# Kernel tuning notes

Hardware: AMD Instinct MI355X
Metric: run time of the kernel (lower is better)

Reference implementation:

```python
import jax, jax.numpy as jnp
import numpy as np

B, S, NX, NH = 2, 2048, 1024, 16
HD = NX // NH  # head dim = 64

def setup_inputs() -> dict:
    key = jax.random.key(0)
    k1, k2, k3 = jax.random.split(key, 3)
    return {
        "x": jax.random.normal(k1, (B, S, NX), dtype=jnp.float32),
        "c_attn_w": jax.random.normal(k2, (NX, 3 * NX), dtype=jnp.float32) * 0.02,
        "c_attn_b": jnp.zeros((3 * NX,), dtype=jnp.float32),
        "c_proj_w": jax.random.normal(k3, (NX, NX), dtype=jnp.float32) * 0.02,
        "c_proj_b": jnp.zeros((NX,), dtype=jnp.float32),
    }

def reference(x, c_attn_w, c_attn_b, c_proj_w, c_proj_b):
    b, s, nx = x.shape
    # fused QKV projection (Conv1D == affine on last dim)
    qkv = x @ c_attn_w + c_attn_b                      # [b, s, 3*nx]
    q, k, v = jnp.split(qkv, 3, axis=-1)
    # split heads -> [b, h, s, d]
    q = q.reshape(b, s, NH, HD).transpose(0, 2, 1, 3)
    k = k.reshape(b, s, NH, HD).transpose(0, 2, 1, 3)
    v = v.reshape(b, s, NH, HD).transpose(0, 2, 1, 3)
    # scaled scores with causal mask (masked_fill -1e10, matching original)
    w = jnp.einsum("bhqd,bhkd->bhqk", q, k) / jnp.sqrt(jnp.float32(HD))
    causal = jnp.tril(jnp.ones((s, s), dtype=bool))    # [s, s]
    w = jnp.where(causal[None, None, :, :], w, jnp.float32(-1e10))
    w = jax.nn.softmax(w, axis=-1)
    a = jnp.einsum("bhqk,bhkd->bhqd", w, v)            # [b, h, s, d]
    # merge heads
    a = a.transpose(0, 2, 1, 3).reshape(b, s, nx)
    # output projection (dropout is identity in eval)
    return a @ c_proj_w + c_proj_b
```

## Files before the change

kernel.cpp:

```cpp
#include <hip/hip_runtime.h>
#include <cstdint>

typedef unsigned short u16;
typedef unsigned int u32;
typedef float f32x4 __attribute__((ext_vector_type(4)));
typedef __bf16 bf16x8 __attribute__((ext_vector_type(8)));
typedef __bf16 bf16x4 __attribute__((ext_vector_type(4)));
typedef u16 u16x8 __attribute__((ext_vector_type(8)));

#define B_ 2
#define S_ 2048
#define NX_ 1024
#define NH_ 16
#define HD_ 64
#define T3_ 3072
#define M_ 4096
#define SCL 0.18033688011112042f

__device__ __forceinline__ u16 bfbits(float f) {
    __bf16 h = (__bf16)f;
    return __builtin_bit_cast(u16, h);
}

__device__ __forceinline__ void gload_lds16(const void* g, void* l) {
    auto gp = reinterpret_cast<const __attribute__((address_space(1))) u32*>(
        reinterpret_cast<uintptr_t>(g));
    auto lp = reinterpret_cast<__attribute__((address_space(3))) u32*>(
        reinterpret_cast<uintptr_t>(l));
    __builtin_amdgcn_global_load_lds(gp, lp, 16, 0, 0);
}

__global__ __launch_bounds__(256) void cvt_bf16_kernel(const float* __restrict__ X,
                                                       u16* __restrict__ Y) {
    int i = (blockIdx.x * 256 + threadIdx.x) * 4;
    float4 v = *reinterpret_cast<const float4*>(X + i);
    bf16x4 o;
    o[0] = (__bf16)v.x; o[1] = (__bf16)v.y; o[2] = (__bf16)v.z; o[3] = (__bf16)v.w;
    *reinterpret_cast<bf16x4*>(Y + i) = o;
}

__global__ __launch_bounds__(256) void transpose_cvt_kernel(const float* __restrict__ W,
                                                            u16* __restrict__ WT,
                                                            int K, int N) {
    __shared__ float tile[32][33];
    int nbx = N >> 5;
    int nb = (blockIdx.x % nbx) << 5;
    int kb = (blockIdx.x / nbx) << 5;
    int tx = threadIdx.x & 31, ty = threadIdx.x >> 5;
#pragma unroll
    for (int i = 0; i < 32; i += 8)
        tile[ty + i][tx] = W[(size_t)(kb + ty + i) * N + nb + tx];
    __syncthreads();
#pragma unroll
    for (int i = 0; i < 32; i += 8)
        WT[(size_t)(nb + ty + i) * K + kb + tx] = bfbits(tile[tx][ty + i]);
}

#define BM 128
#define BN 128
#define BK 64
__global__ __launch_bounds__(256) void gemm_bt_kernel(const u16* __restrict__ A,
                                                      const u16* __restrict__ Bt,
                                                      const float* __restrict__ bias,
                                                      u16* __restrict__ Cb,
                                                      float* __restrict__ Cf,
                                                      u16* __restrict__ Vt,
                                                      int vcol0,
                                                      int M, int N, int K) {
    __shared__ u16 a_lds[BM * BK];
    __shared__ u16 b_lds[BN * BK];
    int nbn = N / BN;
    int nwg = gridDim.x;
    int orig = blockIdx.x;
    int wg = (orig & 7) * (nwg >> 3) + (orig >> 3);
    int bm = wg / nbn, bn = wg % nbn;
    int t = threadIdx.x;
    int w = t >> 6, l = t & 63, lg = l >> 4, lr = l & 15;
    int wr = w >> 1, wc = w & 1;
    const u16* Abase = A + (size_t)bm * BM * K;
    const u16* Bbase = Bt + (size_t)bn * BN * K;

    f32x4 zero4 = {0.f, 0.f, 0.f, 0.f};
    f32x4 acc[4][4];
#pragma unroll
    for (int m = 0; m < 4; ++m)
#pragma unroll
        for (int n = 0; n < 4; ++n) acc[m][n] = zero4;

    int nkt = K / BK;
    for (int kt = 0; kt < nkt; ++kt) {
#pragma unroll
        for (int it = 0; it < 4; ++it) {
            int idx = it * 256 + t;
            int row = idx >> 3, ck = idx & 7;
            int ldsoff = (it * 256 + w * 64) * 8;
            gload_lds16(Abase + (size_t)row * K + kt * BK + ck * 8, a_lds + ldsoff);
            gload_lds16(Bbase + (size_t)row * K + kt * BK + ck * 8, b_lds + ldsoff);
        }
        __syncthreads();
#pragma unroll
        for (int ks = 0; ks < 2; ++ks) {
            bf16x8 af[4], bf[4];
#pragma unroll
            for (int m = 0; m < 4; ++m)
                af[m] = *reinterpret_cast<const bf16x8*>(
                    a_lds + (wr * 64 + m * 16 + lr) * BK + ks * 32 + lg * 8);
#pragma unroll
            for (int n = 0; n < 4; ++n)
                bf[n] = *reinterpret_cast<const bf16x8*>(
                    b_lds + (wc * 64 + n * 16 + lr) * BK + ks * 32 + lg * 8);
#pragma unroll
            for (int m = 0; m < 4; ++m)
#pragma unroll
                for (int n = 0; n < 4; ++n)
                    acc[m][n] = __builtin_amdgcn_mfma_f32_16x16x32_bf16(
                        af[m], bf[n], acc[m][n], 0, 0, 0);
        }
        __syncthreads();
    }
#pragma unroll
    for (int n = 0; n < 4; ++n) {
        int col0 = bn * BN + wc * 64 + n * 16;
        int col = col0 + lr;
        float bv = bias[col];
        bool isv = (Vt != nullptr) && (col0 >= vcol0);
#pragma unroll
        for (int m = 0; m < 4; ++m) {
            int row0 = bm * BM + wr * 64 + m * 16 + lg * 4;
            if (isv) {
                int nv = col - vcol0, hh = nv >> 6, dd = nv & 63;
                int bb = row0 >> 11, ss = row0 & 2047;
                bf16x4 pk;
#pragma unroll
                for (int r = 0; r < 4; ++r) pk[r] = (__bf16)(acc[m][n][r] + bv);
                *reinterpret_cast<bf16x4*>(
                    Vt + (((size_t)(bb * 16 + hh) * 64 + dd) << 11) + ss) = pk;
            } else {
#pragma unroll
                for (int r = 0; r < 4; ++r) {
                    float v = acc[m][n][r] + bv;
                    if (Cf) Cf[(size_t)(row0 + r) * N + col] = v;
                    else    Cb[(size_t)(row0 + r) * N + col] = bfbits(v);
                }
            }
        }
    }
}

__global__ __launch_bounds__(256) void attn_kernel(const u16* __restrict__ qkv,
                                                   const u16* __restrict__ Vt,
                                                   u16* __restrict__ outa) {
    __shared__ u16 k_lds[2][4096];
    __shared__ u16 v_lds[2][4096];
    __shared__ u16 p_lds[4096];

    int bid = blockIdx.x;
    int g = bid & 31;
    int j = bid >> 5;
    int j0 = j & 7, kk = j >> 3;
    int qt = (kk == 0) ? j0 : (kk == 1) ? (31 - j0) : (kk == 2) ? (8 + j0) : (23 - j0);
    int b = g >> 4, h = g & 15;
    int t = threadIdx.x, w = t >> 6, l = t & 63, lg = l >> 4, lr = l & 15;
    const u16* base = qkv + (size_t)b * S_ * T3_;
    const u16* vbase = Vt + (size_t)g * 64 * S_;
    int prow = w * 16 + lr;
    int srow = w * 8 + (l >> 3);
    int qb = qt * 64;
    int qrow = qb + w * 16 + lr;

    auto stage = [&](int kt2, int bs) {
        int kb2 = kt2 * 64;
#pragma unroll
        for (int it = 0; it < 2; ++it) {
            int row = it * 32 + srow;
            int ckg = (l & 7) ^ (row & 7);
            gload_lds16(base + (size_t)(kb2 + row) * T3_ + NX_ + h * 64 + ckg * 8,
                        &k_lds[bs][(it * 32 + w * 8) * 64]);
            gload_lds16(vbase + (size_t)row * S_ + kb2 + ckg * 8,
                        &v_lds[bs][(it * 32 + w * 8) * 64]);
        }
    };

    f32x4 zero4 = {0.f, 0.f, 0.f, 0.f};

    bf16x8 qf[2];
#pragma unroll
    for (int ks = 0; ks < 2; ++ks)
        qf[ks] = *reinterpret_cast<const bf16x8*>(
            base + (size_t)qrow * T3_ + h * 64 + ks * 32 + lg * 8);

    f32x4 oacc[4];
#pragma unroll
    for (int dc = 0; dc < 4; ++dc) oacc[dc] = zero4;
    float mrun = -1e30f, lrun = 0.f;
    int nkt = qt + 1;

    stage(0, 0);
    __syncthreads();

    for (int kt = 0; kt < nkt; ++kt) {
        int cur = kt & 1;
        if (kt + 1 < nkt) stage(kt + 1, cur ^ 1);

        f32x4 sacc[4];
#pragma unroll
        for (int kn = 0; kn < 4; ++kn) sacc[kn] = zero4;
        __builtin_amdgcn_s_setprio(1);
#pragma unroll
        for (int ks = 0; ks < 2; ++ks) {
#pragma unroll
            for (int kn = 0; kn < 4; ++kn) {
                bf16x8 kf = *reinterpret_cast<const bf16x8*>(
                    &k_lds[cur][(kn * 16 + lr) * 64 + (((ks * 4 + lg) ^ (lr & 7)) * 8)]);
                sacc[kn] = __builtin_amdgcn_mfma_f32_16x16x32_bf16(
                    kf, qf[ks], sacc[kn], 0, 0, 0);
            }
        }
        __builtin_amdgcn_s_setprio(0);

        if (kt == qt) {
            int qloc = w * 16 + lr;
#pragma unroll
            for (int kn = 0; kn < 4; ++kn)
#pragma unroll
                for (int r = 0; r < 4; ++r)
                    if (kn * 16 + lg * 4 + r > qloc) sacc[kn][r] = -1e30f;
        }

        float mx = -1e30f;
#pragma unroll
        for (int kn = 0; kn < 4; ++kn) {
            float a0 = fmaxf(sacc[kn][0], sacc[kn][1]);
            float a1 = fmaxf(sacc[kn][2], sacc[kn][3]);
            mx = fmaxf(mx, fmaxf(a0, a1));
        }
        mx = fmaxf(mx, __shfl_xor(mx, 16));
        mx = fmaxf(mx, __shfl_xor(mx, 32));

        bool noresc = __all(mx <= mrun + 8.0f);
        float mnew = noresc ? mrun : fmaxf(mrun, mx);

        float rs = 0.f;
#pragma unroll
        for (int kn = 0; kn < 4; ++kn)
#pragma unroll
            for (int r = 0; r < 4; ++r) {
                float pv = exp2f((sacc[kn][r] - mnew) * SCL);
                sacc[kn][r] = pv;
                rs += pv;
            }
        rs += __shfl_xor(rs, 16);
        rs += __shfl_xor(rs, 32);

        if (noresc) {
            lrun += rs;
        } else {
            float fsc = exp2f((mrun - mnew) * SCL);
            mrun = mnew;
            lrun = lrun * fsc + rs;
            float f0 = __shfl(fsc, lg * 4 + 0);
            float f1 = __shfl(fsc, lg * 4 + 1);
            float f2 = __shfl(fsc, lg * 4 + 2);
            float f3 = __shfl(fsc, lg * 4 + 3);
#pragma unroll
            for (int dc = 0; dc < 4; ++dc) {
                oacc[dc][0] *= f0; oacc[dc][1] *= f1;
                oacc[dc][2] *= f2; oacc[dc][3] *= f3;
            }
        }

#pragma unroll
        for (int kn = 0; kn < 4; ++kn) {
            bf16x4 pb;
            pb[0] = (__bf16)sacc[kn][0]; pb[1] = (__bf16)sacc[kn][1];
            pb[2] = (__bf16)sacc[kn][2]; pb[3] = (__bf16)sacc[kn][3];
            int byteoff = prow * 128 + (((2 * kn + (lg >> 1)) ^ (prow & 7)) * 16) + (lg & 1) * 8;
            *reinterpret_cast<bf16x4*>(reinterpret_cast<char*>(p_lds) + byteoff) = pb;
        }

        __builtin_amdgcn_s_setprio(1);
#pragma unroll
        for (int ks = 0; ks < 2; ++ks) {
            bf16x8 pf = *reinterpret_cast<const bf16x8*>(
                reinterpret_cast<char*>(p_lds) + prow * 128 + (((ks * 4 + lg) ^ (prow & 7)) * 16));
#pragma unroll
            for (int dc = 0; dc < 4; ++dc) {
                bf16x8 vf = *reinterpret_cast<const bf16x8*>(
                    &v_lds[cur][(dc * 16 + lr) * 64 + (((ks * 4 + lg) ^ (lr & 7)) * 8)]);
                oacc[dc] = __builtin_amdgcn_mfma_f32_16x16x32_bf16(
                    pf, vf, oacc[dc], 0, 0, 0);
            }
        }
        __builtin_amdgcn_s_setprio(0);
        __syncthreads();
    }

    float inv = 1.f / lrun;
    float i0 = __shfl(inv, lg * 4 + 0);
    float i1 = __shfl(inv, lg * 4 + 1);
    float i2 = __shfl(inv, lg * 4 + 2);
    float i3 = __shfl(inv, lg * 4 + 3);
    u16* ob = outa + (size_t)b * S_ * NX_;
#pragma unroll
    for (int r = 0; r < 4; ++r) {
        float ir = (r == 0) ? i0 : (r == 1) ? i1 : (r == 2) ? i2 : i3;
        int row = qb + w * 16 + lg * 4 + r;
#pragma unroll
        for (int dc = 0; dc < 4; ++dc)
            ob[(size_t)row * NX_ + h * 64 + dc * 16 + lr] = bfbits(oacc[dc][r] * ir);
    }
}

extern "C" void kernel_launch(void* const* d_in, const int* in_sizes, int n_in,
                              void* d_out, int out_size, void* d_ws, size_t ws_size,
                              hipStream_t stream) {
    const float* x        = (const float*)d_in[0];
    const float* c_attn_w = (const float*)d_in[1];
    const float* c_attn_b = (const float*)d_in[2];
    const float* c_proj_w = (const float*)d_in[3];
    const float* c_proj_b = (const float*)d_in[4];
    float* out = (float*)d_out;

    u16* xb     = (u16*)d_ws;
    u16* wqkvT  = xb + (size_t)M_ * NX_;
    u16* wprojT = wqkvT + (size_t)T3_ * NX_;
    u16* qkv    = wprojT + (size_t)NX_ * NX_;
    u16* attno  = xb;
    u16* Vtp    = (u16*)d_out;

    cvt_bf16_kernel<<<(M_ * NX_) / 1024, 256, 0, stream>>>(x, xb);
    transpose_cvt_kernel<<<(T3_ / 32) * (NX_ / 32), 256, 0, stream>>>(c_attn_w, wqkvT, NX_, T3_);
    transpose_cvt_kernel<<<(NX_ / 32) * (NX_ / 32), 256, 0, stream>>>(c_proj_w, wprojT, NX_, NX_);
    gemm_bt_kernel<<<(M_ / BM) * (T3_ / BN), 256, 0, stream>>>(
        xb, wqkvT, c_attn_b, qkv, nullptr, Vtp, 2 * NX_, M_, T3_, NX_);
    attn_kernel<<<1024, 256, 0, stream>>>(qkv, Vtp, attno);
    gemm_bt_kernel<<<(M_ / BM) * (NX_ / BN), 256, 0, stream>>>(
        attno, wprojT, c_proj_b, nullptr, out, nullptr, 0, M_, NX_, NX_);
}
```

Measured before the change: 127.9 us.

## Rewrite attention with 32x32x16 MFMA, 128-row query tiles, register P exchange

The attention kernel now gives each block a 128-row query tile, with each wave owning 32 rows, and uses 32x32x16 bf16 MFMA for both QK^T and PV. The P matrix is repacked in registers with lane shuffles instead of a round trip through LDS, which removes the p_lds buffer. Each K/V tile loaded into LDS is now reused by twice as many query rows, and the grid is halved with a simpler causal tile ordering. In exchange, waves with fewer causal tiles sit idle in the later iterations while still hitting the barriers, and register pressure rises with the larger accumulators.

```diff
diff --git a/kernel.cpp b/kernel.cpp
--- a/kernel.cpp
+++ b/kernel.cpp
@@ -4,9 +4,12 @@
 typedef unsigned short u16;
 typedef unsigned int u32;
 typedef float f32x4 __attribute__((ext_vector_type(4)));
+typedef float f32x16 __attribute__((ext_vector_type(16)));
 typedef __bf16 bf16x8 __attribute__((ext_vector_type(8)));
 typedef __bf16 bf16x4 __attribute__((ext_vector_type(4)));
+typedef __bf16 bf16x2 __attribute__((ext_vector_type(2)));
 typedef u16 u16x8 __attribute__((ext_vector_type(8)));
+typedef u32 u32x4 __attribute__((ext_vector_type(4)));
 
 #define B_ 2
 #define S_ 2048
@@ -20,6 +23,10 @@
 __device__ __forceinline__ u16 bfbits(float f) {
     __bf16 h = (__bf16)f;
     return __builtin_bit_cast(u16, h);
+}
+__device__ __forceinline__ u32 pk2(float a, float b) {
+    bf16x2 t; t[0] = (__bf16)a; t[1] = (__bf16)b;
+    return __builtin_bit_cast(u32, t);
 }
 
 __device__ __forceinline__ void gload_lds16(const void* g, void* l) {
@@ -152,21 +159,19 @@
                                                    u16* __restrict__ outa) {
     __shared__ u16 k_lds[2][4096];
     __shared__ u16 v_lds[2][4096];
-    __shared__ u16 p_lds[4096];
 
     int bid = blockIdx.x;
     int g = bid & 31;
     int j = bid >> 5;
-    int j0 = j & 7, kk = j >> 3;
-    int qt = (kk == 0) ? j0 : (kk == 1) ? (31 - j0) : (kk == 2) ? (8 + j0) : (23 - j0);
+    int qt = (j < 8) ? (15 - j) : (j - 8);
     int b = g >> 4, h = g & 15;
-    int t = threadIdx.x, w = t >> 6, l = t & 63, lg = l >> 4, lr = l & 15;
+    int t = threadIdx.x, w = t >> 6, l = t & 63;
+    int c31 = l & 31, hi = l >> 5;
     const u16* base = qkv + (size_t)b * S_ * T3_;
     const u16* vbase = Vt + (size_t)g * 64 * S_;
-    int prow = w * 16 + lr;
     int srow = w * 8 + (l >> 3);
-    int qb = qt * 64;
-    int qrow = qb + w * 16 + lr;
+    int qb = qt * 128 + w * 32;
+    int q = qb + c31;
 
     auto stage = [&](int kt2, int bs) {
         int kb2 = kt2 * 64;
@@ -181,19 +186,21 @@
         }
     };
 
-    f32x4 zero4 = {0.f, 0.f, 0.f, 0.f};
-
-    bf16x8 qf[2];
-#pragma unroll
-    for (int ks = 0; ks < 2; ++ks)
+    bf16x8 qf[4];
+#pragma unroll
+    for (int ks = 0; ks < 4; ++ks)
         qf[ks] = *reinterpret_cast<const bf16x8*>(
-            base + (size_t)qrow * T3_ + h * 64 + ks * 32 + lg * 8);
-
-    f32x4 oacc[4];
-#pragma unroll
-    for (int dc = 0; dc < 4; ++dc) oacc[dc] = zero4;
+            base + (size_t)q * T3_ + h * 64 + ks * 16 + hi * 8);
+
+    f32x16 oacc[2];
+#pragma unroll
+    for (int dc = 0; dc < 2; ++dc)
+#pragma unroll
+        for (int r = 0; r < 16; ++r) oacc[dc][r] = 0.f;
     float mrun = -1e30f, lrun = 0.f;
-    int nkt = qt + 1;
+
+    int nkt = 2 * qt + 2;
+    int tw = 2 * qt + (w >> 1);
 
     stage(0, 0);
     __syncthreads();
@@ -202,112 +209,121 @@
         int cur = kt & 1;
         if (kt + 1 < nkt) stage(kt + 1, cur ^ 1);
 
-        f32x4 sacc[4];
-#pragma unroll
-        for (int kn = 0; kn < 4; ++kn) sacc[kn] = zero4;
-        __builtin_amdgcn_s_setprio(1);
-#pragma unroll
-        for (int ks = 0; ks < 2; ++ks) {
-#pragma unroll
-            for (int kn = 0; kn < 4; ++kn) {
-                bf16x8 kf = *reinterpret_cast<const bf16x8*>(
-                    &k_lds[cur][(kn * 16 + lr) * 64 + (((ks * 4 + lg) ^ (lr & 7)) * 8)]);
-                sacc[kn] = __builtin_amdgcn_mfma_f32_16x16x32_bf16(
-                    kf, qf[ks], sacc[kn], 0, 0, 0);
-            }
-        }
-        __builtin_amdgcn_s_setprio(0);
-
-        if (kt == qt) {
-            int qloc = w * 16 + lr;
-#pragma unroll
-            for (int kn = 0; kn < 4; ++kn)
-#pragma unroll
-                for (int r = 0; r < 4; ++r)
-                    if (kn * 16 + lg * 4 + r > qloc) sacc[kn][r] = -1e30f;
-        }
-
-        float mx = -1e30f;
-#pragma unroll
-        for (int kn = 0; kn < 4; ++kn) {
-            float a0 = fmaxf(sacc[kn][0], sacc[kn][1]);
-            float a1 = fmaxf(sacc[kn][2], sacc[kn][3]);
-            mx = fmaxf(mx, fmaxf(a0, a1));
-        }
-        mx = fmaxf(mx, __shfl_xor(mx, 16));
-        mx = fmaxf(mx, __shfl_xor(mx, 32));
-
-        bool noresc = __all(mx <= mrun + 8.0f);
-        float mnew = noresc ? mrun : fmaxf(mrun, mx);
-
-        float rs = 0.f;
-#pragma unroll
-        for (int kn = 0; kn < 4; ++kn)
-#pragma unroll
-            for (int r = 0; r < 4; ++r) {
-                float pv = exp2f((sacc[kn][r] - mnew) * SCL);
-                sacc[kn][r] = pv;
-                rs += pv;
-            }
-        rs += __shfl_xor(rs, 16);
-        rs += __shfl_xor(rs, 32);
-
-        if (noresc) {
-            lrun += rs;
-        } else {
-            float fsc = exp2f((mrun - mnew) * SCL);
-            mrun = mnew;
-            lrun = lrun * fsc + rs;
-            float f0 = __shfl(fsc, lg * 4 + 0);
-            float f1 = __shfl(fsc, lg * 4 + 1);
-            float f2 = __shfl(fsc, lg * 4 + 2);
-            float f3 = __shfl(fsc, lg * 4 + 3);
-#pragma unroll
-            for (int dc = 0; dc < 4; ++dc) {
-                oacc[dc][0] *= f0; oacc[dc][1] *= f1;
-                oacc[dc][2] *= f2; oacc[dc][3] *= f3;
-            }
-        }
-
-#pragma unroll
-        for (int kn = 0; kn < 4; ++kn) {
-            bf16x4 pb;
-            pb[0] = (__bf16)sacc[kn][0]; pb[1] = (__bf16)sacc[kn][1];
-            pb[2] = (__bf16)sacc[kn][2]; pb[3] = (__bf16)sacc[kn][3];
-            int byteoff = prow * 128 + (((2 * kn + (lg >> 1)) ^ (prow & 7)) * 16) + (lg & 1) * 8;
-            *reinterpret_cast<bf16x4*>(reinterpret_cast<char*>(p_lds) + byteoff) = pb;
-        }
-
-        __builtin_amdgcn_s_setprio(1);
-#pragma unroll
-        for (int ks = 0; ks < 2; ++ks) {
-            bf16x8 pf = *reinterpret_cast<const bf16x8*>(
-                reinterpret_cast<char*>(p_lds) + prow * 128 + (((ks * 4 + lg) ^ (prow & 7)) * 16));
-#pragma unroll
-            for (int dc = 0; dc < 4; ++dc) {
-                bf16x8 vf = *reinterpret_cast<const bf16x8*>(
-                    &v_lds[cur][(dc * 16 + lr) * 64 + (((ks * 4 + lg) ^ (lr & 7)) * 8)]);
-                oacc[dc] = __builtin_amdgcn_mfma_f32_16x16x32_bf16(
-                    pf, vf, oacc[dc], 0, 0, 0);
-            }
-        }
-        __builtin_amdgcn_s_setprio(0);
+        if (kt <= tw) {
+            int kb = kt * 64;
+            f32x16 sacc[2];
+#pragma unroll
+            for (int kn = 0; kn < 2; ++kn)
+#pragma unroll
+                for (int r = 0; r < 16; ++r) sacc[kn][r] = 0.f;
+            __builtin_amdgcn_s_setprio(1);
+#pragma unroll
+            for (int ks = 0; ks < 4; ++ks) {
+#pragma unroll
+                for (int kn = 0; kn < 2; ++kn) {
+                    int row = kn * 32 + c31;
+                    int ck = (ks * 2 + hi) ^ (row & 7);
+                    bf16x8 kf = *reinterpret_cast<const bf16x8*>(
+                        &k_lds[cur][row * 64 + ck * 8]);
+                    sacc[kn] = __builtin_amdgcn_mfma_f32_32x32x16_bf16(
+                        kf, qf[ks], sacc[kn], 0, 0, 0);
+                }
+            }
+            __builtin_amdgcn_s_setprio(0);
+
+            if (kt == tw) {
+#pragma unroll
+                for (int kn = 0; kn < 2; ++kn)
+#pragma unroll
+                    for (int r = 0; r < 16; ++r) {
+                        int kv = kb + kn * 32 + (r & 3) + 8 * (r >> 2) + 4 * hi;
+                        if (kv > q) sacc[kn][r] = -1e30f;
+                    }
+            }
+
+            float mx = -1e30f;
+#pragma unroll
+            for (int kn = 0; kn < 2; ++kn)
+#pragma unroll
+                for (int r = 0; r < 16; ++r) mx = fmaxf(mx, sacc[kn][r]);
+            mx = fmaxf(mx, __shfl_xor(mx, 32));
+
+            bool noresc = __all(mx <= mrun + 8.0f);
+            float mnew = noresc ? mrun : fmaxf(mrun, mx);
+
+            float rs = 0.f;
+#pragma unroll
+            for (int kn = 0; kn < 2; ++kn)
+#pragma unroll
+                for (int r = 0; r < 16; ++r) {
+                    float pv = exp2f((sacc[kn][r] - mnew) * SCL);
+                    sacc[kn][r] = pv;
+                    rs += pv;
+                }
+            rs += __shfl_xor(rs, 32);
+
+            if (noresc) {
+                lrun += rs;
+            } else {
+                float fsc = exp2f((mrun - mnew) * SCL);
+                mrun = mnew;
+                lrun = lrun * fsc + rs;
+#pragma unroll
+                for (int r = 0; r < 16; ++r) {
+                    int cr = (r & 3) + 8 * (r >> 2) + 4 * hi;
+                    float f = __shfl(fsc, cr);
+                    oacc[0][r] *= f; oacc[1][r] *= f;
+                }
+            }
+
+            __builtin_amdgcn_s_setprio(1);
+#pragma unroll
+            for (int kn = 0; kn < 2; ++kn) {
+                u32 a0 = pk2(sacc[kn][0],  sacc[kn][1]),  a1 = pk2(sacc[kn][2],  sacc[kn][3]);
+                u32 b0 = pk2(sacc[kn][4],  sacc[kn][5]),  b1 = pk2(sacc[kn][6],  sacc[kn][7]);
+                u32 c0 = pk2(sacc[kn][8],  sacc[kn][9]),  c1 = pk2(sacc[kn][10], sacc[kn][11]);
+                u32 d0 = pk2(sacc[kn][12], sacc[kn][13]), d1 = pk2(sacc[kn][14], sacc[kn][15]);
+                u32 pa0 = __shfl_xor(a0, 32), pa1 = __shfl_xor(a1, 32);
+                u32 pb0 = __shfl_xor(b0, 32), pb1 = __shfl_xor(b1, 32);
+                u32 pc0 = __shfl_xor(c0, 32), pc1 = __shfl_xor(c1, 32);
+                u32 pd0 = __shfl_xor(d0, 32), pd1 = __shfl_xor(d1, 32);
+                u32x4 f0, f1;
+                f0[0] = hi ? pb0 : a0;  f0[1] = hi ? pb1 : a1;
+                f0[2] = hi ? b0 : pa0;  f0[3] = hi ? b1 : pa1;
+                f1[0] = hi ? pd0 : c0;  f1[1] = hi ? pd1 : c1;
+                f1[2] = hi ? d0 : pc0;  f1[3] = hi ? d1 : pc1;
+                bf16x8 pf0 = __builtin_bit_cast(bf16x8, f0);
+                bf16x8 pf1 = __builtin_bit_cast(bf16x8, f1);
+#pragma unroll
+                for (int dc = 0; dc < 2; ++dc) {
+                    int d = dc * 32 + c31;
+                    int ck0 = ((kn * 2 + 0) * 2 + hi) ^ (d & 7);
+                    int ck1 = ((kn * 2 + 1) * 2 + hi) ^ (d & 7);
+                    bf16x8 vf0 = *reinterpret_cast<const bf16x8*>(
+                        &v_lds[cur][d * 64 + ck0 * 8]);
+                    oacc[dc] = __builtin_amdgcn_mfma_f32_32x32x16_bf16(
+                        pf0, vf0, oacc[dc], 0, 0, 0);
+                    bf16x8 vf1 = *reinterpret_cast<const bf16x8*>(
+                        &v_lds[cur][d * 64 + ck1 * 8]);
+                    oacc[dc] = __builtin_amdgcn_mfma_f32_32x32x16_bf16(
+                        pf1, vf1, oacc[dc], 0, 0, 0);
+                }
+            }
+            __builtin_amdgcn_s_setprio(0);
+        }
         __syncthreads();
     }
 
     float inv = 1.f / lrun;
-    float i0 = __shfl(inv, lg * 4 + 0);
-    float i1 = __shfl(inv, lg * 4 + 1);
-    float i2 = __shfl(inv, lg * 4 + 2);
-    float i3 = __shfl(inv, lg * 4 + 3);
     u16* ob = outa + (size_t)b * S_ * NX_;
 #pragma unroll
-    for (int r = 0; r < 4; ++r) {
-        float ir = (r == 0) ? i0 : (r == 1) ? i1 : (r == 2) ? i2 : i3;
-        int row = qb + w * 16 + lg * 4 + r;
-#pragma unroll
-        for (int dc = 0; dc < 4; ++dc)
-            ob[(size_t)row * NX_ + h * 64 + dc * 16 + lr] = bfbits(oacc[dc][r] * ir);
+    for (int r = 0; r < 16; ++r) {
+        int cr = (r & 3) + 8 * (r >> 2) + 4 * hi;
+        float iv = __shfl(inv, cr);
+        int row = qb + cr;
+#pragma unroll
+        for (int dc = 0; dc < 2; ++dc)
+            ob[(size_t)row * NX_ + h * 64 + dc * 32 + c31] = bfbits(oacc[dc][r] * iv);
     }
 }
 
@@ -333,7 +349,7 @@
     transpose_cvt_kernel<<<(NX_ / 32) * (NX_ / 32), 256, 0, stream>>>(c_proj_w, wprojT, NX_, NX_);
     gemm_bt_kernel<<<(M_ / BM) * (T3_ / BN), 256, 0, stream>>>(
         xb, wqkvT, c_attn_b, qkv, nullptr, Vtp, 2 * NX_, M_, T3_, NX_);
-    attn_kernel<<<1024, 256, 0, stream>>>(qkv, Vtp, attno);
+    attn_kernel<<<512, 256, 0, stream>>>(qkv, Vtp, attno);
     gemm_bt_kernel<<<(M_ / BM) * (NX_ / BN), 256, 0, stream>>>(
         attno, wprojT, c_proj_b, nullptr, out, nullptr, 0, M_, NX_, NX_);
 }
```

Measured after the change: 138.9 us. +8.6%, slower.

## Split causal attention KV range across two blocks and merge partial results

Applied to the files above, without the earlier changes.

Each query tile's key range is now split into two halves handled by separate blocks, doubling the attention grid. Tiles are scheduled longest-first. Each block writes unnormalized partial outputs plus its running max and sum into spare workspace regions. A new merge kernel rescales and combines the two partials into the final attention output. The aim is shorter per-block critical paths and better CU balance across the causal triangle, paid for with an extra kernel launch and extra global memory traffic for the partials.

```diff
diff --git a/kernel.cpp b/kernel.cpp
--- a/kernel.cpp
+++ b/kernel.cpp
@@ -149,7 +149,9 @@
 
 __global__ __launch_bounds__(256) void attn_kernel(const u16* __restrict__ qkv,
                                                    const u16* __restrict__ Vt,
-                                                   u16* __restrict__ outa) {
+                                                   u16* __restrict__ part0,
+                                                   u16* __restrict__ part1,
+                                                   float* __restrict__ mlb) {
     __shared__ u16 k_lds[2][4096];
     __shared__ u16 v_lds[2][4096];
     __shared__ u16 p_lds[4096];
@@ -157,8 +159,8 @@
     int bid = blockIdx.x;
     int g = bid & 31;
     int j = bid >> 5;
-    int j0 = j & 7, kk = j >> 3;
-    int qt = (kk == 0) ? j0 : (kk == 1) ? (31 - j0) : (kk == 2) ? (8 + j0) : (23 - j0);
+    int qt = 31 - (j >> 1);
+    int s = j & 1;
     int b = g >> 4, h = g & 15;
     int t = threadIdx.x, w = t >> 6, l = t & 63, lg = l >> 4, lr = l & 15;
     const u16* base = qkv + (size_t)b * S_ * T3_;
@@ -168,6 +170,11 @@
     int qb = qt * 64;
     int qrow = qb + w * 16 + lr;
 
+    int nt = qt + 1;
+    int h1 = (nt + 1) >> 1;
+    int k0 = s ? h1 : 0;
+    int k1 = s ? nt : h1;
+
     auto stage = [&](int kt2, int bs) {
         int kb2 = kt2 * 64;
 #pragma unroll
@@ -193,14 +200,13 @@
 #pragma unroll
     for (int dc = 0; dc < 4; ++dc) oacc[dc] = zero4;
     float mrun = -1e30f, lrun = 0.f;
-    int nkt = qt + 1;
-
-    stage(0, 0);
+
+    if (k0 < k1) stage(k0, 0);
     __syncthreads();
 
-    for (int kt = 0; kt < nkt; ++kt) {
-        int cur = kt & 1;
-        if (kt + 1 < nkt) stage(kt + 1, cur ^ 1);
+    for (int kt = k0; kt < k1; ++kt) {
+        int cur = (kt - k0) & 1;
+        if (kt + 1 < k1) stage(kt + 1, cur ^ 1);
 
         f32x4 sacc[4];
 #pragma unroll
@@ -295,19 +301,42 @@
         __syncthreads();
     }
 
-    float inv = 1.f / lrun;
-    float i0 = __shfl(inv, lg * 4 + 0);
-    float i1 = __shfl(inv, lg * 4 + 1);
-    float i2 = __shfl(inv, lg * 4 + 2);
-    float i3 = __shfl(inv, lg * 4 + 3);
-    u16* ob = outa + (size_t)b * S_ * NX_;
+    u16* pb = (s ? part1 : part0) + (size_t)b * S_ * NX_;
 #pragma unroll
     for (int r = 0; r < 4; ++r) {
-        float ir = (r == 0) ? i0 : (r == 1) ? i1 : (r == 2) ? i2 : i3;
         int row = qb + w * 16 + lg * 4 + r;
 #pragma unroll
         for (int dc = 0; dc < 4; ++dc)
-            ob[(size_t)row * NX_ + h * 64 + dc * 16 + lr] = bfbits(oacc[dc][r] * ir);
+            pb[(size_t)row * NX_ + h * 64 + dc * 16 + lr] = bfbits(oacc[dc][r]);
+    }
+    if (lg == 0) {
+        float* f = mlb + (size_t)(b * S_ + qrow) * (T3_ / 2) + (NX_ / 2) * 2 + h * 4 + s * 2;
+        f[0] = mrun; f[1] = lrun;
+    }
+}
+
+__global__ __launch_bounds__(256) void merge_kernel(u16* __restrict__ part0,
+                                                    const u16* __restrict__ part1,
+                                                    const float* __restrict__ mlb) {
+    int idx = blockIdx.x * 256 + threadIdx.x;
+    int tok = idx >> 4, h = idx & 15;
+    const float* f = mlb + (size_t)tok * (T3_ / 2) + (NX_ / 2) * 2 + h * 4;
+    float m0 = f[0], l0 = f[1], m1 = f[2], l1 = f[3];
+    float M = fmaxf(m0, m1);
+    float e0 = exp2f((m0 - M) * SCL), e1 = exp2f((m1 - M) * SCL);
+    float inv = 1.f / (l0 * e0 + l1 * e1);
+    float a = e0 * inv, c = e1 * inv;
+    u16* p0 = part0 + (size_t)tok * NX_ + h * 64;
+    const u16* p1 = part1 + (size_t)tok * NX_ + h * 64;
+#pragma unroll
+    for (int i = 0; i < 8; ++i) {
+        bf16x8 v0 = *reinterpret_cast<const bf16x8*>(p0 + i * 8);
+        bf16x8 v1 = *reinterpret_cast<const bf16x8*>(p1 + i * 8);
+        bf16x8 o;
+#pragma unroll
+        for (int k = 0; k < 8; ++k)
+            o[k] = (__bf16)((float)v0[k] * a + (float)v1[k] * c);
+        *reinterpret_cast<bf16x8*>(p0 + i * 8) = o;
     }
 }
 
@@ -327,13 +356,16 @@
     u16* qkv    = wprojT + (size_t)NX_ * NX_;
     u16* attno  = xb;
     u16* Vtp    = (u16*)d_out;
+    u16* part1  = Vtp + (size_t)32 * 64 * S_;
+    float* mlb  = (float*)qkv;
 
     cvt_bf16_kernel<<<(M_ * NX_) / 1024, 256, 0, stream>>>(x, xb);
     transpose_cvt_kernel<<<(T3_ / 32) * (NX_ / 32), 256, 0, stream>>>(c_attn_w, wqkvT, NX_, T3_);
     transpose_cvt_kernel<<<(NX_ / 32) * (NX_ / 32), 256, 0, stream>>>(c_proj_w, wprojT, NX_, NX_);
     gemm_bt_kernel<<<(M_ / BM) * (T3_ / BN), 256, 0, stream>>>(
         xb, wqkvT, c_attn_b, qkv, nullptr, Vtp, 2 * NX_, M_, T3_, NX_);
-    attn_kernel<<<1024, 256, 0, stream>>>(qkv, Vtp, attno);
+    attn_kernel<<<2048, 256, 0, stream>>>(qkv, Vtp, attno, part1, mlb);
+    merge_kernel<<<(M_ * NH_) / 256, 256, 0, stream>>>(attno, part1, mlb);
     gemm_bt_kernel<<<(M_ / BM) * (NX_ / BN), 256, 0, stream>>>(
         attno, wprojT, c_proj_b, nullptr, out, nullptr, 0, M_, NX_, NX_);
 }
```

After: 132.7 us. +3.8%, slower.

## Load K and V fragments directly from global memory instead of staging through LDS

Applied to the files above, without the earlier changes.

The attention kernel drops its double-buffered LDS staging of K and V tiles. Each wave now reads its MFMA fragments straight from global memory (relying on L2/L1 caching) and removes the per-iteration block barrier. Launch bounds are raised to request higher occupancy. The trade is that each of the four waves redundantly fetches the same K/V tiles and there is no explicit prefetch, so global-load latency is exposed inside the loop.

```diff
diff --git a/kernel.cpp b/kernel.cpp
--- a/kernel.cpp
+++ b/kernel.cpp
@@ -147,11 +147,9 @@
     }
 }
 
-__global__ __launch_bounds__(256) void attn_kernel(const u16* __restrict__ qkv,
-                                                   const u16* __restrict__ Vt,
-                                                   u16* __restrict__ outa) {
-    __shared__ u16 k_lds[2][4096];
-    __shared__ u16 v_lds[2][4096];
+__global__ __launch_bounds__(256, 4) void attn_kernel(const u16* __restrict__ qkv,
+                                                      const u16* __restrict__ Vt,
+                                                      u16* __restrict__ outa) {
     __shared__ u16 p_lds[4096];
 
     int bid = blockIdx.x;
@@ -164,22 +162,11 @@
     const u16* base = qkv + (size_t)b * S_ * T3_;
     const u16* vbase = Vt + (size_t)g * 64 * S_;
     int prow = w * 16 + lr;
-    int srow = w * 8 + (l >> 3);
     int qb = qt * 64;
     int qrow = qb + w * 16 + lr;
 
-    auto stage = [&](int kt2, int bs) {
-        int kb2 = kt2 * 64;
-#pragma unroll
-        for (int it = 0; it < 2; ++it) {
-            int row = it * 32 + srow;
-            int ckg = (l & 7) ^ (row & 7);
-            gload_lds16(base + (size_t)(kb2 + row) * T3_ + NX_ + h * 64 + ckg * 8,
-                        &k_lds[bs][(it * 32 + w * 8) * 64]);
-            gload_lds16(vbase + (size_t)row * S_ + kb2 + ckg * 8,
-                        &v_lds[bs][(it * 32 + w * 8) * 64]);
-        }
-    };
+    const u16* kptr = base + (size_t)lr * T3_ + NX_ + h * 64 + lg * 8;
+    const u16* vptr = vbase + (size_t)lr * S_ + lg * 8;
 
     f32x4 zero4 = {0.f, 0.f, 0.f, 0.f};
 
@@ -195,28 +182,36 @@
     float mrun = -1e30f, lrun = 0.f;
     int nkt = qt + 1;
 
-    stage(0, 0);
-    __syncthreads();
-
     for (int kt = 0; kt < nkt; ++kt) {
-        int cur = kt & 1;
-        if (kt + 1 < nkt) stage(kt + 1, cur ^ 1);
+        int kb = kt * 64;
+
+        bf16x8 kf[2][4];
+#pragma unroll
+        for (int ks = 0; ks < 2; ++ks)
+#pragma unroll
+            for (int kn = 0; kn < 4; ++kn)
+                kf[ks][kn] = *reinterpret_cast<const bf16x8*>(
+                    kptr + (size_t)(kb + kn * 16) * T3_ + ks * 32);
 
         f32x4 sacc[4];
 #pragma unroll
         for (int kn = 0; kn < 4; ++kn) sacc[kn] = zero4;
         __builtin_amdgcn_s_setprio(1);
 #pragma unroll
-        for (int ks = 0; ks < 2; ++ks) {
-#pragma unroll
-            for (int kn = 0; kn < 4; ++kn) {
-                bf16x8 kf = *reinterpret_cast<const bf16x8*>(
-                    &k_lds[cur][(kn * 16 + lr) * 64 + (((ks * 4 + lg) ^ (lr & 7)) * 8)]);
+        for (int ks = 0; ks < 2; ++ks)
+#pragma unroll
+            for (int kn = 0; kn < 4; ++kn)
                 sacc[kn] = __builtin_amdgcn_mfma_f32_16x16x32_bf16(
-                    kf, qf[ks], sacc[kn], 0, 0, 0);
-            }
-        }
+                    kf[ks][kn], qf[ks], sacc[kn], 0, 0, 0);
         __builtin_amdgcn_s_setprio(0);
+
+        bf16x8 vf[2][4];
+#pragma unroll
+        for (int ks = 0; ks < 2; ++ks)
+#pragma unroll
+            for (int dc = 0; dc < 4; ++dc)
+                vf[ks][dc] = *reinterpret_cast<const bf16x8*>(
+                    vptr + (size_t)(dc * 16) * S_ + kb + ks * 32);
 
         if (kt == qt) {
             int qloc = w * 16 + lr;
@@ -284,15 +279,11 @@
             bf16x8 pf = *reinterpret_cast<const bf16x8*>(
                 reinterpret_cast<char*>(p_lds) + prow * 128 + (((ks * 4 + lg) ^ (prow & 7)) * 16));
 #pragma unroll
-            for (int dc = 0; dc < 4; ++dc) {
-                bf16x8 vf = *reinterpret_cast<const bf16x8*>(
-                    &v_lds[cur][(dc * 16 + lr) * 64 + (((ks * 4 + lg) ^ (lr & 7)) * 8)]);
+            for (int dc = 0; dc < 4; ++dc)
                 oacc[dc] = __builtin_amdgcn_mfma_f32_16x16x32_bf16(
-                    pf, vf, oacc[dc], 0, 0, 0);
-            }
+                    pf, vf[ks][dc], oacc[dc], 0, 0, 0);
         }
         __builtin_amdgcn_s_setprio(0);
-        __syncthreads();
     }
 
     float inv = 1.f / lrun;
```

Result: slower. 199.9 us (+56.3%).
